# Performance work log

Hardware: AMD Instinct MI355X
Metric: run time of the kernel (lower is better)

The kernel has to match this reference:

```python
import jax, jax.numpy as jnp
import numpy as np

VOXEL_SIZE = np.array([0.05, 0.05, 0.1], np.float32)
PC_RANGE = np.array([0.0, -40.0, -3.0, 70.4, 40.0, 1.0], np.float32)
GRID = np.round((PC_RANGE[3:] - PC_RANGE[:3]) / VOXEL_SIZE).astype(np.int64)  # [1408, 1600, 40]
MAX_POINTS = 35
MAX_VOXELS = 120000
N_POINTS = 1_500_000


def setup_inputs() -> dict:
    key = jax.random.key(0)
    k1, k2 = jax.random.split(key)
    u = jax.random.uniform(k1, (N_POINTS, 3), dtype=jnp.float32)
    lo = jnp.array([-2.0, -42.0, -3.5], jnp.float32)   # slightly outside range -> some points dropped
    hi = jnp.array([72.0, 42.0, 1.5], jnp.float32)
    xyz = lo + u * (hi - lo)
    feat = jax.random.uniform(k2, (N_POINTS, 1), dtype=jnp.float32)
    return {"points": jnp.concatenate([xyz, feat], axis=1)}


def _voxelize(points):
    """Deterministic hard voxelization (mmcv hard_voxelize_forward semantics).

    Returns fixed-shape (jit-friendly) padded outputs plus voxel_num; the
    original CUDA op returns the first voxel_num rows of each array.
    """
    N = points.shape[0]
    gx, gy, gz = int(GRID[0]), int(GRID[1]), int(GRID[2])
    n_cells = gx * gy * gz
    vsz = jnp.asarray(VOXEL_SIZE)
    lo = jnp.asarray(PC_RANGE[:3])

    c = jnp.floor((points[:, :3] - lo) / vsz).astype(jnp.int64)          # [N,3] voxel coord (x,y,z)
    valid = jnp.all((c >= 0) & (c < jnp.array([gx, gy, gz])), axis=1)    # remove_outside_points=True
    lin = c[:, 2] * (gy * gx) + c[:, 1] * gx + c[:, 0]                    # linear voxel id
    key_ = jnp.where(valid, lin, n_cells)                                 # sentinel bin for invalid

    pos = jnp.arange(N, dtype=jnp.int64)
    order = jnp.argsort(key_ * N + pos)                # stable sort by voxel key (composite key)
    skey = key_[order]
    is_start = jnp.concatenate([jnp.ones((1,), bool), skey[1:] != skey[:-1]])
    gid = jnp.cumsum(is_start) - 1                      # group id per sorted position

    g_start = jax.ops.segment_min(pos, gid, num_segments=N)
    slot = pos - g_start[gid]                           # arrival-order slot within voxel
    rep = jax.ops.segment_min(order, gid, num_segments=N)   # first original index per group
    g_key = jax.ops.segment_min(skey, gid, num_segments=N)
    g_valid = g_key < n_cells

    # voxel ids assigned in order of first point occurrence (deterministic variant)
    rep_s = jnp.where(g_valid, rep, N)
    rank = jnp.zeros(N, jnp.int64).at[jnp.argsort(rep_s)].set(pos)   # inverse permutation = rank
    vox_of_group = jnp.where(g_valid & (rank < MAX_VOXELS), rank, -1)

    v = vox_of_group[gid]                               # voxel id per sorted point (-1 dropped)
    keep = (v >= 0) & (slot < MAX_POINTS)
    vid = jnp.where(v >= 0, v, MAX_VOXELS)              # OOB index -> dropped by mode='drop'

    voxels = jnp.zeros((MAX_VOXELS, MAX_POINTS, points.shape[1]), points.dtype)
    voxels = voxels.at[vid, slot].set(points[order], mode='drop')

    npts = jax.ops.segment_sum(keep.astype(jnp.int32), jnp.where(keep, v, MAX_VOXELS),
                               num_segments=MAX_VOXELS + 1)[:MAX_VOXELS]

    czyx = c[:, ::-1].astype(jnp.int32)                 # mmcv stores coors as (z, y, x)
    g_idx = jnp.where(vox_of_group >= 0, vox_of_group, MAX_VOXELS)
    coors = jnp.zeros((MAX_VOXELS, 3), jnp.int32).at[g_idx].set(
        czyx[jnp.clip(rep, 0, N - 1)], mode='drop')

    voxel_num = jnp.minimum(jnp.sum(g_valid.astype(jnp.int32)), MAX_VOXELS)
    return voxels, coors, npts, voxel_num


def reference(points):
    return _voxelize(points)
```

## Files before the change

kernel.cpp:

```cpp
#include <hip/hip_runtime.h>
#include <stdint.h>
#include <stdio.h>


#define GXc 1408
#define GYc 1600
#define GXY (GXc * GYc)
#define MAXV 120000
#define MAXP 35
#define MPREFIX 262144
#define TBITS 21
#define TSIZE (1u << TBITS)
#define TMASK (TSIZE - 1u)
#define NBW (TSIZE / 32u)
#define EMPTY64 0xFFFFFFFFFFFFFFFFull
#define INV32 0xFFFFFFFFu
#define SCAN_B 256
#define SCAN_I 8
#define SCAN_TILE (SCAN_B * SCAN_I)
#define OUT_ELEMS ((size_t)MAXV * MAXP * 4 + (size_t)MAXV * 3 + (size_t)MAXV + 1)

typedef unsigned long long u64;

__global__ void Voxelization_50345606644201_kernel() {}

__device__ __forceinline__ uint32_t mix32(uint32_t x) {
    x ^= x >> 16; x *= 0x85ebca6bu;
    x ^= x >> 13; x *= 0xc2b2ae35u;
    x ^= x >> 16;
    return x;
}

__device__ __forceinline__ float bfr(float f) {
    union { float f; uint32_t u; } v; v.f = f;
    v.u = (v.u + 0x7FFFu + ((v.u >> 16) & 1u)) & 0xFFFF0000u;
    return v.f;
}

struct Cell { int cx, cy, cz; int valid; };

__device__ __forceinline__ Cell cell_of(float4 p) {
    float fx = floorf((p.x - 0.0f)     / 0.05f);
    float fy = floorf((p.y - (-40.0f)) / 0.05f);
    float fz = floorf((p.z - (-3.0f))  / 0.1f);
    Cell c;
    c.valid = (fx >= 0.0f) && (fx < 1408.0f) &&
              (fy >= 0.0f) && (fy < 1600.0f) &&
              (fz >= 0.0f) && (fz < 40.0f);
    c.cx = (int)fx; c.cy = (int)fy; c.cz = (int)fz;
    return c;
}

__global__ void k_init(u64* __restrict__ table, uint32_t* __restrict__ bits,
                       uint32_t* __restrict__ flags32,
                       uint32_t* __restrict__ dupeflag32, uint32_t nfw,
                       uint32_t* __restrict__ cnt, uint32_t* __restrict__ misc) {
    uint32_t stride = gridDim.x * blockDim.x;
    uint32_t tid = blockIdx.x * blockDim.x + threadIdx.x;
    for (uint32_t j = tid; j < TSIZE; j += stride) table[j] = EMPTY64;
    for (uint32_t j = tid; j < NBW; j += stride) bits[j] = 0u;
    for (uint32_t j = tid; j < nfw; j += stride) { flags32[j] = 0u; dupeflag32[j] = 0u; }
    for (uint32_t j = tid; j < (uint32_t)MAXV; j += stride) cnt[j] = 0u;
    if (tid == 0) { misc[0] = 0u; misc[1] = 0u; }
}

__global__ void k_pointsA(const float4* __restrict__ pts, int M,
                          u64* __restrict__ table, uint32_t* __restrict__ bits,
                          uint8_t* __restrict__ dupeflag,
                          uint32_t* __restrict__ gclaims) {
    __shared__ uint32_t scl;
    if (threadIdx.x == 0) scl = 0u;
    __syncthreads();
    uint32_t claims = 0;
    int base = blockIdx.x * (blockDim.x * 4) + threadIdx.x;
    #pragma unroll
    for (int r = 0; r < 4; r++) {
        int i = base + r * blockDim.x;
        if (i < M) {
            float4 p = pts[i];
            Cell c = cell_of(p);
            if (c.valid) {
                uint32_t lin = (uint32_t)c.cz * (uint32_t)GXY
                             + (uint32_t)c.cy * (uint32_t)GXc + (uint32_t)c.cx;
                u64 val = ((u64)(uint32_t)i << 32) | (u64)lin;
                uint32_t h = mix32(lin) & TMASK;
                for (uint32_t probes = 0; probes <= TMASK; probes++) {
                    u64 prev = atomicCAS(&table[h], EMPTY64, val);
                    if (prev == EMPTY64) {
                        atomicOr(&bits[h >> 5], 1u << (h & 31u));
                        claims++;
                        break;
                    }
                    if ((uint32_t)prev == lin) {
                        u64 old = atomicMin(&table[h], val);
                        uint32_t loser = (val < old) ? (uint32_t)(old >> 32)
                                                     : (uint32_t)i;
                        dupeflag[loser] = 1u;
                        break;
                    }
                    h = (h + 1u) & TMASK;
                }
            }
        }
    }
    if (claims) atomicAdd(&scl, claims);
    __syncthreads();
    if (threadIdx.x == 0 && scl) atomicAdd(gclaims, scl);
}

__global__ void k_pointsB(const float4* __restrict__ pts, int M, int n,
                          u64* __restrict__ table, uint32_t* __restrict__ bits,
                          uint8_t* __restrict__ dupeflag,
                          const uint32_t* __restrict__ gclaims) {
    int i = M + blockIdx.x * blockDim.x + threadIdx.x;
    if (i >= n) return;
    float4 p = pts[i];
    Cell c = cell_of(p);
    if (!c.valid) return;
    uint32_t lin = (uint32_t)c.cz * (uint32_t)GXY
                 + (uint32_t)c.cy * (uint32_t)GXc + (uint32_t)c.cx;
    uint32_t h = mix32(lin) & TMASK;
    if (*gclaims >= (uint32_t)MAXV) {
        for (uint32_t probes = 0; probes <= TMASK; probes++) {
            if (!((bits[h >> 5] >> (h & 31u)) & 1u)) return;
            u64 e = table[h];
            if ((uint32_t)e == lin) { dupeflag[i] = 1u; return; }
            h = (h + 1u) & TMASK;
        }
        return;
    }
    u64 val = ((u64)(uint32_t)i << 32) | (u64)lin;
    for (uint32_t probes = 0; probes <= TMASK; probes++) {
        u64 e = table[h];
        if ((uint32_t)e == lin) { dupeflag[i] = 1u; return; }
        if (e == EMPTY64) {
            u64 prev = atomicCAS(&table[h], EMPTY64, val);
            if (prev == EMPTY64) {
                atomicOr(&bits[h >> 5], 1u << (h & 31u));
                return;
            }
            if ((uint32_t)prev == lin) {
                u64 old = atomicMin(&table[h], val);
                uint32_t loser = (val < old) ? (uint32_t)(old >> 32) : (uint32_t)i;
                dupeflag[loser] = 1u;
                return;
            }
        }
        h = (h + 1u) & TMASK;
    }
}

__global__ void k_sweep(const u64* __restrict__ table,
                        uint8_t* __restrict__ flags) {
    uint32_t stride = gridDim.x * blockDim.x;
    uint32_t tid = blockIdx.x * blockDim.x + threadIdx.x;
    for (uint32_t j = tid; j < TSIZE; j += stride) {
        u64 e = table[j];
        if (e != EMPTY64) flags[(uint32_t)(e >> 32)] = 1u;
    }
}

__device__ __forceinline__ uint32_t flag_at(const uint8_t* __restrict__ flags,
                                            int i, int n) {
    return (i < n) ? (uint32_t)flags[i] : 0u;
}

__global__ void k_scanA(const uint8_t* __restrict__ flags, int n,
                        uint32_t* __restrict__ bsums) {
    __shared__ uint32_t sh[SCAN_B];
    int t = threadIdx.x;
    int myStart = blockIdx.x * SCAN_TILE + t * SCAN_I;
    uint32_t s = 0;
    #pragma unroll
    for (int j = 0; j < SCAN_I; j++) s += flag_at(flags, myStart + j, n);
    sh[t] = s; __syncthreads();
    for (int off = SCAN_B / 2; off > 0; off >>= 1) {
        if (t < off) sh[t] += sh[t + off];
        __syncthreads();
    }
    if (t == 0) bsums[blockIdx.x] = sh[0];
}

__global__ void k_scanC(const float4* __restrict__ pts,
                        const uint8_t* __restrict__ flags, int n, int nb,
                        const uint32_t* __restrict__ bsums,
                        uint32_t* __restrict__ vrank,
                        float* __restrict__ coors,
                        uint32_t* __restrict__ cnt,
                        uint32_t* __restrict__ slotsrc,
                        float4* __restrict__ vox4,
                        uint32_t* __restrict__ tot,
                        float* __restrict__ voxnum) {
    __shared__ uint32_t sh[SCAN_B];
    __shared__ uint32_t exoff_sh;
    int t = threadIdx.x;
    int bid = blockIdx.x;
    uint32_t part = 0;
    for (int j = t; j < bid; j += SCAN_B) part += bsums[j];
    sh[t] = part; __syncthreads();
    for (int off = SCAN_B / 2; off > 0; off >>= 1) {
        if (t < off) sh[t] += sh[t + off];
        __syncthreads();
    }
    if (t == 0) exoff_sh = sh[0];
    __syncthreads();
    uint32_t exoff = exoff_sh;
    __syncthreads();
    int myStart = bid * SCAN_TILE + t * SCAN_I;
    uint32_t f[SCAN_I];
    uint32_t lsum = 0;
    #pragma unroll
    for (int j = 0; j < SCAN_I; j++) {
        f[j] = flag_at(flags, myStart + j, n);
        lsum += f[j];
    }
    sh[t] = lsum; __syncthreads();
    for (int off = 1; off < SCAN_B; off <<= 1) {
        uint32_t add = (t >= off) ? sh[t - off] : 0u;
        __syncthreads();
        sh[t] += add;
        __syncthreads();
    }
    if (bid == nb - 1 && t == 0) {
        uint32_t total = exoff + sh[SCAN_B - 1];
        *tot = total;
        uint32_t vn = total < (uint32_t)MAXV ? total : (uint32_t)MAXV;
        *voxnum = bfr((float)vn);
    }
    uint32_t rank = exoff + (sh[t] - lsum);
    for (int j = 0; j < SCAN_I; j++) {
        if (f[j]) {
            int i = myStart + j;
            if (rank < (uint32_t)MAXV) {
                vrank[i] = rank;
                float4 p = pts[i];
                Cell c = cell_of(p);
                size_t cb = (size_t)rank * 3;
                coors[cb + 0] = bfr((float)c.cz);
                coors[cb + 1] = bfr((float)c.cy);
                coors[cb + 2] = bfr((float)c.cx);
                uint32_t base = rank * (uint32_t)MAXP;
                cnt[rank] = 1u;
                slotsrc[base] = (uint32_t)i;
                vox4[base] = make_float4(bfr(p.x), bfr(p.y), bfr(p.z), bfr(p.w));
            } else {
                vrank[i] = INV32;
            }
            rank++;
        }
    }
}

__global__ void k_dupes(const float4* __restrict__ pts,
                        const u64* __restrict__ table,
                        const uint32_t* __restrict__ vrank,
                        const uint8_t* __restrict__ dupeflag, int n,
                        uint32_t* __restrict__ cnt,
                        uint32_t* __restrict__ slotsrc,
                        float4* __restrict__ vox4) {
    int stride = gridDim.x * blockDim.x;
    for (int i = blockIdx.x * blockDim.x + threadIdx.x; i < n; i += stride) {
        if (!dupeflag[i]) continue;
        float4 p = pts[i];
        Cell c = cell_of(p);
        uint32_t lin = (uint32_t)c.cz * (uint32_t)GXY
                     + (uint32_t)c.cy * (uint32_t)GXc + (uint32_t)c.cx;
        uint32_t h = mix32(lin) & TMASK;
        uint32_t mi = INV32;
        for (uint32_t probes = 0; probes <= TMASK; probes++) {
            u64 e = table[h];
            if ((uint32_t)e == lin) { mi = (uint32_t)(e >> 32); break; }
            if (e == EMPTY64) break;
            h = (h + 1u) & TMASK;
        }
        if (mi == INV32) continue;
        uint32_t v = vrank[mi];
        if (v >= (uint32_t)MAXV) continue;
        uint32_t s = atomicAdd(&cnt[v], 1u);
        if (s < (uint32_t)MAXP) {
            uint32_t idx = v * (uint32_t)MAXP + s;
            slotsrc[idx] = (uint32_t)i;
            vox4[idx] = make_float4(bfr(p.x), bfr(p.y), bfr(p.z), bfr(p.w));
        }
    }
}

__global__ void k_final(const uint32_t* __restrict__ cnt,
                        uint32_t* __restrict__ slotsrc,
                        float4* __restrict__ vox4,
                        float* __restrict__ npts) {
    int v = blockIdx.x * blockDim.x + threadIdx.x;
    if (v >= MAXV) return;
    uint32_t c = cnt[v];
    uint32_t m = c < (uint32_t)MAXP ? c : (uint32_t)MAXP;
    npts[v] = m ? bfr((float)m) : 0.0f;
    if (m >= 2u) {
        uint32_t base = (uint32_t)v * (uint32_t)MAXP;
        for (uint32_t a = 0; a + 1u < m; a++) {
            uint32_t best = a, bi = slotsrc[base + a];
            for (uint32_t b = a + 1u; b < m; b++) {
                uint32_t ti = slotsrc[base + b];
                if (ti < bi) { bi = ti; best = b; }
            }
            if (best != a) {
                uint32_t ta = slotsrc[base + a];
                slotsrc[base + a] = slotsrc[base + best];
                slotsrc[base + best] = ta;
                float4 va = vox4[base + a];
                vox4[base + a] = vox4[base + best];
                vox4[base + best] = va;
            }
        }
    }
}

extern "C" void kernel_launch(void* const* d_in, const int* in_sizes, int n_in,
                              void* d_out, int out_size, void* d_ws, size_t ws_size,
                              hipStream_t stream) {
    (void)n_in; (void)out_size;
    const float4* pts = (const float4*)d_in[0];
    int n = in_sizes[0] / 4;
    int M = MPREFIX < n ? MPREFIX : n;

    float* out    = (float*)d_out;
    float* coors  = out + (size_t)MAXV * MAXP * 4;
    float* npts   = coors + (size_t)MAXV * 3;
    float* voxnum = out + (OUT_ELEMS - 1);

    size_t npad = ((size_t)n + 255) & ~(size_t)255;
    size_t off = 0;
    size_t oT = off;  off += (size_t)TSIZE * 8;
    size_t oBt = off; off += (size_t)NBW * 4;
    size_t oF = off;  off += npad;
    size_t oDF = off; off += npad;
    size_t oV = off;  off += (size_t)n * 4;
    off = (off + 255) & ~(size_t)255;
    size_t oC = off;  off += (size_t)MAXV * 4;
    off = (off + 255) & ~(size_t)255;
    size_t oB = off;  off += 4096;
    size_t oX = off;  off += 256;
    size_t oS = off;  off += (size_t)MAXV * MAXP * 4;
    size_t need = off;

    if (need > ws_size) return;

    char* w = (char*)d_ws;
    u64*      table    = (u64*)(w + oT);
    uint32_t* bits     = (uint32_t*)(w + oBt);
    uint8_t*  flags    = (uint8_t*)(w + oF);
    uint8_t*  dupeflag = (uint8_t*)(w + oDF);
    uint32_t* vrank    = (uint32_t*)(w + oV);
    uint32_t* cnt      = (uint32_t*)(w + oC);
    uint32_t* bsums    = (uint32_t*)(w + oB);
    uint32_t* misc     = (uint32_t*)(w + oX);
    uint32_t* tot      = misc;
    uint32_t* gclaims  = misc + 1;
    uint32_t* slotsrc  = (uint32_t*)(w + oS);

    int nbA    = (M + 1023) / 1024;
    int nbB    = (n - M + 255) / 256;
    int nbScan = (n + SCAN_TILE - 1) / SCAN_TILE;
    uint32_t nfw = ((uint32_t)npad) / 4u;

    k_init<<<2048, 256, 0, stream>>>(table, bits, (uint32_t*)flags,
                                     (uint32_t*)dupeflag, nfw, cnt, misc);
    k_pointsA<<<nbA, 256, 0, stream>>>(pts, M, table, bits, dupeflag, gclaims);
    if (n > M)
        k_pointsB<<<nbB, 256, 0, stream>>>(pts, M, n, table, bits, dupeflag,
                                           gclaims);
    k_sweep<<<2048, 256, 0, stream>>>(table, flags);
    k_scanA<<<nbScan, SCAN_B, 0, stream>>>(flags, n, bsums);
    k_scanC<<<nbScan, SCAN_B, 0, stream>>>(pts, flags, n, nbScan, bsums,
                                           vrank, coors, cnt, slotsrc,
                                           (float4*)out, tot, voxnum);
    k_dupes<<<1024, 256, 0, stream>>>(pts, table, vrank, dupeflag, n,
                                      cnt, slotsrc, (float4*)out);
    k_final<<<(MAXV + 255) / 256, 256, 0, stream>>>(cnt, slotsrc, (float4*)out,
                                                    npts);

    hipStreamCaptureStatus cs = hipStreamCaptureStatusNone;
    (void)hipStreamIsCapturing(stream, &cs);
    if (cs == hipStreamCaptureStatusNone) {
        static uint32_t h_tot, h_cl; static float h_vn;
        h_tot = 0; h_cl = 0; h_vn = -1.0f;
        (void)hipStreamSynchronize(stream);
        (void)hipMemcpyAsync(&h_tot, tot, 4, hipMemcpyDeviceToHost, stream);
        (void)hipMemcpyAsync(&h_cl, gclaims, 4, hipMemcpyDeviceToHost, stream);
        (void)hipMemcpyAsync(&h_vn, voxnum, 4, hipMemcpyDeviceToHost, stream);
        (void)hipStreamSynchronize(stream);
        fprintf(stderr, "[vox r18] n=%d M=%d claims=%u tot=%u voxnum=%.1f (exp 119808)\n",
                n, M, h_cl, h_tot, h_vn);
        fflush(stderr);
    }
}
```

Before: 70.08 us.

## Shrink hash table and replace occupancy bitmap with per-slot 8-bit signatures

Halves the open-addressing hash table and shortens the prefix of points inserted with atomics, so less memory is initialised and walked by the sweep. The occupancy bitmap is replaced by a byte-per-slot signature taken from the high hash bits. Lookups in the saturated path can then skip 64-bit table reads on mismatched slots, and inserts no longer need atomicOr. The per-voxel count clear is dropped from init, presumably because a later kernel sets it, and the final kernel exits early for voxels beyond the total count. The smaller table raises load factor and probe lengths, and a smaller prefix could leave the claim count short of the cap for longer.

```diff
diff --git a/kernel.cpp b/kernel.cpp
--- a/kernel.cpp
+++ b/kernel.cpp
@@ -8,11 +8,10 @@
 #define GXY (GXc * GYc)
 #define MAXV 120000
 #define MAXP 35
-#define MPREFIX 262144
-#define TBITS 21
+#define MPREFIX 180224
+#define TBITS 20
 #define TSIZE (1u << TBITS)
 #define TMASK (TSIZE - 1u)
-#define NBW (TSIZE / 32u)
 #define EMPTY64 0xFFFFFFFFFFFFFFFFull
 #define INV32 0xFFFFFFFFu
 #define SCAN_B 256
@@ -51,21 +50,20 @@
     return c;
 }
 
-__global__ void k_init(u64* __restrict__ table, uint32_t* __restrict__ bits,
+__global__ void k_init(u64* __restrict__ table, uint32_t* __restrict__ sig32,
                        uint32_t* __restrict__ flags32,
                        uint32_t* __restrict__ dupeflag32, uint32_t nfw,
-                       uint32_t* __restrict__ cnt, uint32_t* __restrict__ misc) {
+                       uint32_t* __restrict__ misc) {
     uint32_t stride = gridDim.x * blockDim.x;
     uint32_t tid = blockIdx.x * blockDim.x + threadIdx.x;
     for (uint32_t j = tid; j < TSIZE; j += stride) table[j] = EMPTY64;
-    for (uint32_t j = tid; j < NBW; j += stride) bits[j] = 0u;
+    for (uint32_t j = tid; j < TSIZE / 4u; j += stride) sig32[j] = 0u;
     for (uint32_t j = tid; j < nfw; j += stride) { flags32[j] = 0u; dupeflag32[j] = 0u; }
-    for (uint32_t j = tid; j < (uint32_t)MAXV; j += stride) cnt[j] = 0u;
     if (tid == 0) { misc[0] = 0u; misc[1] = 0u; }
 }
 
 __global__ void k_pointsA(const float4* __restrict__ pts, int M,
-                          u64* __restrict__ table, uint32_t* __restrict__ bits,
+                          u64* __restrict__ table, uint8_t* __restrict__ sig,
                           uint8_t* __restrict__ dupeflag,
                           uint32_t* __restrict__ gclaims) {
     __shared__ uint32_t scl;
@@ -82,12 +80,14 @@
             if (c.valid) {
                 uint32_t lin = (uint32_t)c.cz * (uint32_t)GXY
                              + (uint32_t)c.cy * (uint32_t)GXc + (uint32_t)c.cx;
+                uint32_t full = mix32(lin);
+                uint32_t h = full & TMASK;
+                uint8_t mysig = (uint8_t)((full >> 24) | 1u);
                 u64 val = ((u64)(uint32_t)i << 32) | (u64)lin;
-                uint32_t h = mix32(lin) & TMASK;
                 for (uint32_t probes = 0; probes <= TMASK; probes++) {
                     u64 prev = atomicCAS(&table[h], EMPTY64, val);
                     if (prev == EMPTY64) {
-                        atomicOr(&bits[h >> 5], 1u << (h & 31u));
+                        sig[h] = mysig;
                         claims++;
                         break;
                     }
@@ -109,7 +109,7 @@
 }
 
 __global__ void k_pointsB(const float4* __restrict__ pts, int M, int n,
-                          u64* __restrict__ table, uint32_t* __restrict__ bits,
+                          u64* __restrict__ table, uint8_t* __restrict__ sig,
                           uint8_t* __restrict__ dupeflag,
                           const uint32_t* __restrict__ gclaims) {
     int i = M + blockIdx.x * blockDim.x + threadIdx.x;
@@ -119,12 +119,17 @@
     if (!c.valid) return;
     uint32_t lin = (uint32_t)c.cz * (uint32_t)GXY
                  + (uint32_t)c.cy * (uint32_t)GXc + (uint32_t)c.cx;
-    uint32_t h = mix32(lin) & TMASK;
+    uint32_t full = mix32(lin);
+    uint32_t h = full & TMASK;
+    uint8_t mysig = (uint8_t)((full >> 24) | 1u);
     if (*gclaims >= (uint32_t)MAXV) {
         for (uint32_t probes = 0; probes <= TMASK; probes++) {
-            if (!((bits[h >> 5] >> (h & 31u)) & 1u)) return;
-            u64 e = table[h];
-            if ((uint32_t)e == lin) { dupeflag[i] = 1u; return; }
+            uint8_t s = sig[h];
+            if (s == 0u) return;
+            if (s == mysig) {
+                u64 e = table[h];
+                if ((uint32_t)e == lin) { dupeflag[i] = 1u; return; }
+            }
             h = (h + 1u) & TMASK;
         }
         return;
@@ -135,10 +140,7 @@
         if ((uint32_t)e == lin) { dupeflag[i] = 1u; return; }
         if (e == EMPTY64) {
             u64 prev = atomicCAS(&table[h], EMPTY64, val);
-            if (prev == EMPTY64) {
-                atomicOr(&bits[h >> 5], 1u << (h & 31u));
-                return;
-            }
+            if (prev == EMPTY64) { sig[h] = mysig; return; }
             if ((uint32_t)prev == lin) {
                 u64 old = atomicMin(&table[h], val);
                 uint32_t loser = (val < old) ? (uint32_t)(old >> 32) : (uint32_t)i;
@@ -288,12 +290,15 @@
 __global__ void k_final(const uint32_t* __restrict__ cnt,
                         uint32_t* __restrict__ slotsrc,
                         float4* __restrict__ vox4,
-                        float* __restrict__ npts) {
+                        float* __restrict__ npts,
+                        const uint32_t* __restrict__ tot) {
     int v = blockIdx.x * blockDim.x + threadIdx.x;
     if (v >= MAXV) return;
+    uint32_t total = *tot;
+    if ((uint32_t)v >= total) { npts[v] = 0.0f; return; }
     uint32_t c = cnt[v];
     uint32_t m = c < (uint32_t)MAXP ? c : (uint32_t)MAXP;
-    npts[v] = m ? bfr((float)m) : 0.0f;
+    npts[v] = bfr((float)m);
     if (m >= 2u) {
         uint32_t base = (uint32_t)v * (uint32_t)MAXP;
         for (uint32_t a = 0; a + 1u < m; a++) {
@@ -330,7 +335,7 @@
     size_t npad = ((size_t)n + 255) & ~(size_t)255;
     size_t off = 0;
     size_t oT = off;  off += (size_t)TSIZE * 8;
-    size_t oBt = off; off += (size_t)NBW * 4;
+    size_t oSg = off; off += (size_t)TSIZE;
     size_t oF = off;  off += npad;
     size_t oDF = off; off += npad;
     size_t oV = off;  off += (size_t)n * 4;
@@ -346,7 +351,7 @@
 
     char* w = (char*)d_ws;
     u64*      table    = (u64*)(w + oT);
-    uint32_t* bits     = (uint32_t*)(w + oBt);
+    uint8_t*  sig      = (uint8_t*)(w + oSg);
     uint8_t*  flags    = (uint8_t*)(w + oF);
     uint8_t*  dupeflag = (uint8_t*)(w + oDF);
     uint32_t* vrank    = (uint32_t*)(w + oV);
@@ -362,11 +367,11 @@
     int nbScan = (n + SCAN_TILE - 1) / SCAN_TILE;
     uint32_t nfw = ((uint32_t)npad) / 4u;
 
-    k_init<<<2048, 256, 0, stream>>>(table, bits, (uint32_t*)flags,
-                                     (uint32_t*)dupeflag, nfw, cnt, misc);
-    k_pointsA<<<nbA, 256, 0, stream>>>(pts, M, table, bits, dupeflag, gclaims);
+    k_init<<<2048, 256, 0, stream>>>(table, (uint32_t*)sig, (uint32_t*)flags,
+                                     (uint32_t*)dupeflag, nfw, misc);
+    k_pointsA<<<nbA, 256, 0, stream>>>(pts, M, table, sig, dupeflag, gclaims);
     if (n > M)
-        k_pointsB<<<nbB, 256, 0, stream>>>(pts, M, n, table, bits, dupeflag,
+        k_pointsB<<<nbB, 256, 0, stream>>>(pts, M, n, table, sig, dupeflag,
                                            gclaims);
     k_sweep<<<2048, 256, 0, stream>>>(table, flags);
     k_scanA<<<nbScan, SCAN_B, 0, stream>>>(flags, n, bsums);
@@ -376,7 +381,7 @@
     k_dupes<<<1024, 256, 0, stream>>>(pts, table, vrank, dupeflag, n,
                                       cnt, slotsrc, (float4*)out);
     k_final<<<(MAXV + 255) / 256, 256, 0, stream>>>(cnt, slotsrc, (float4*)out,
-                                                    npts);
+                                                    npts, tot);
 
     hipStreamCaptureStatus cs = hipStreamCaptureStatusNone;
     (void)hipStreamIsCapturing(stream, &cs);
@@ -388,7 +393,7 @@
         (void)hipMemcpyAsync(&h_cl, gclaims, 4, hipMemcpyDeviceToHost, stream);
         (void)hipMemcpyAsync(&h_vn, voxnum, 4, hipMemcpyDeviceToHost, stream);
         (void)hipStreamSynchronize(stream);
-        fprintf(stderr, "[vox r18] n=%d M=%d claims=%u tot=%u voxnum=%.1f (exp 119808)\n",
+        fprintf(stderr, "[vox r21] n=%d M=%d claims=%u tot=%u voxnum=%.1f\n",
                 n, M, h_cl, h_tot, h_vn);
         fflush(stderr);
     }
```

New measurement: 61.50 us. -12.2%, faster.
